# Performance work log

Hardware: AMD Instinct MI355X
Metric: run time of the kernel (lower is better)

## Reference

```python
import jax, jax.numpy as jnp
import numpy as np
import math

B, LA, LB, H = 64, 512, 512, 768


def setup_inputs() -> dict:
    key = jax.random.key(0)
    k1, k2 = jax.random.split(key)
    a = jax.random.normal(k1, (B, LA, H), dtype=jnp.float32)
    b = jax.random.normal(k2, (B, LB, H), dtype=jnp.float32)
    mask_a = jnp.ones((B, LA, 1), dtype=jnp.int32)
    mask_b = jnp.ones((B, LB, 1), dtype=jnp.int32)
    temperature = jnp.asarray(1.0 / math.sqrt(H), dtype=jnp.float32)
    return {"a": a, "b": b, "mask_a": mask_a, "mask_b": mask_b,
            "temperature": temperature}


def reference(a, b, mask_a, mask_b, temperature):
    # attn[b, i, j] = <a_i, b_j> * temperature   -> [B, LA, LB]
    attn = jnp.einsum('bih,bjh->bij', a, b) * temperature
    # pair mask: valid where both positions valid
    mask = jnp.einsum('bik,bjk->bij', mask_a.astype(jnp.float32),
                      mask_b.astype(jnp.float32)) > 0
    NEG = jnp.float32(-1e7)
    attn = jnp.where(mask, attn, NEG)
    attn_a = jax.nn.softmax(attn, axis=1)  # softmax over LA (columns normalize)
    attn_b = jax.nn.softmax(attn, axis=2)  # softmax over LB (rows normalize)
    feature_b = jnp.einsum('bij,bih->bjh', attn_a, a)  # [B, LB, H]
    feature_a = jnp.einsum('bij,bjh->bih', attn_b, b)  # [B, LA, H]
    return feature_a, feature_b
```

## Files before the change

### kernel.cpp

```cpp
#include <hip/hip_runtime.h>
#include <stdint.h>

typedef _Float16 f16;
typedef _Float16 half8_t __attribute__((ext_vector_type(8)));
typedef _Float16 half4_t __attribute__((ext_vector_type(4)));
typedef float floatx4 __attribute__((ext_vector_type(4)));

#define B_  64
#define LA_ 512
#define LB_ 512
#define H_  768

static __device__ __forceinline__ int swz(int row, int byteInRow) {
    return row * 128 + (byteInRow ^ ((row & 7) << 4));
}

__global__ __launch_bounds__(256) void qk_kernel(
    const float* __restrict__ Ag, const float* __restrict__ Bg,
    const int* __restrict__ maskA, const int* __restrict__ maskB,
    const float* __restrict__ temp_p,
    f16* __restrict__ P, f16* __restrict__ PT)
{
    __shared__ f16 As[128 * 64];
    __shared__ f16 Bs[128 * 64];
    __shared__ int mA[128];
    __shared__ int mB[128];

    const int t    = threadIdx.x;
    const int lane = t & 63;
    const int w    = t >> 6;
    const int wm   = w >> 1, wn = w & 1;
    const int jb   = blockIdx.x * 128;
    const int ib   = blockIdx.y * 128;
    const int b    = blockIdx.z;

    if (t < 128)      mA[t]       = maskA[b * LA_ + ib + t];
    else              mB[t - 128] = maskB[b * LB_ + jb + (t - 128)];

    floatx4 acc[4][4] = {};

    const int row  = t >> 1;
    const int half = t & 1;
    const float* srcA = Ag + (size_t)(b * LA_ + ib + row) * H_ + half * 32;
    const float* srcB = Bg + (size_t)(b * LB_ + jb + row) * H_ + half * 32;
    char* AsB = (char*)As;
    char* BsB = (char*)Bs;

    for (int kt = 0; kt < H_ / 64; ++kt) {
        floatx4 a4[8], b4[8];
        const floatx4* pa = (const floatx4*)(srcA + kt * 64);
        const floatx4* pb = (const floatx4*)(srcB + kt * 64);
        #pragma unroll
        for (int q = 0; q < 8; ++q) { a4[q] = pa[q]; b4[q] = pb[q]; }

        __syncthreads();
        #pragma unroll
        for (int q = 0; q < 4; ++q) {
            half8_t ha, hb;
            #pragma unroll
            for (int e = 0; e < 8; ++e) {
                ha[e] = (f16)(a4[2 * q + (e >> 2)][e & 3]);
                hb[e] = (f16)(b4[2 * q + (e >> 2)][e & 3]);
            }
            const int off = swz(row, (half * 4 + q) * 16);
            *(half8_t*)(AsB + off) = ha;
            *(half8_t*)(BsB + off) = hb;
        }
        __syncthreads();

        #pragma unroll
        for (int ks = 0; ks < 2; ++ks) {
            half8_t af[4], bf[4];
            #pragma unroll
            for (int m = 0; m < 4; ++m) {
                const int r = wm * 64 + m * 16 + (lane & 15);
                af[m] = *(half8_t*)(AsB + swz(r, ks * 64 + ((lane >> 4) << 4)));
            }
            #pragma unroll
            for (int n = 0; n < 4; ++n) {
                const int r = wn * 64 + n * 16 + (lane & 15);
                bf[n] = *(half8_t*)(BsB + swz(r, ks * 64 + ((lane >> 4) << 4)));
            }
            #pragma unroll
            for (int m = 0; m < 4; ++m)
                #pragma unroll
                for (int n = 0; n < 4; ++n)
                    acc[m][n] = __builtin_amdgcn_mfma_f32_16x16x32_f16(
                        af[m], bf[n], acc[m][n], 0, 0, 0);
        }
    }

    const float temp = *temp_p;
    #pragma unroll
    for (int m = 0; m < 4; ++m) {
        const int iloc0 = wm * 64 + m * 16 + ((lane >> 4) << 2);
        #pragma unroll
        for (int n = 0; n < 4; ++n) {
            const int jloc = wn * 64 + n * 16 + (lane & 15);
            const int vb = mB[jloc];
            half4_t hv;
            #pragma unroll
            for (int r = 0; r < 4; ++r) {
                const int iloc = iloc0 + r;
                const float s = acc[m][n][r] * temp;
                const float p = (mA[iloc] && vb) ? __expf(s) : 0.0f;
                hv[r] = (f16)p;
                P[(size_t)(b * LA_ + ib + iloc) * LB_ + jb + jloc] = hv[r];
            }
            *(half4_t*)(PT + (size_t)(b * LB_ + jb + jloc) * LA_ + ib + iloc0) = hv;
        }
    }
}

__global__ __launch_bounds__(256) void rowsum_kernel(
    const f16* __restrict__ P, const f16* __restrict__ PT,
    float* __restrict__ lrow, float* __restrict__ lcol)
{
    const int dir = blockIdx.z;
    const f16* src = dir ? PT : P;
    float*     dst = dir ? lcol : lrow;
    const int b  = blockIdx.y;
    const int rb = blockIdx.x * 64;
    const int wv = threadIdx.x >> 6, lane = threadIdx.x & 63;

    for (int r = wv; r < 64; r += 4) {
        const int row = rb + r;
        const half8_t raw = *(const half8_t*)(src + (size_t)(b * 512 + row) * 512 + lane * 8);
        float s = 0.f;
        #pragma unroll
        for (int e = 0; e < 8; ++e) s += (float)raw[e];
        #pragma unroll
        for (int off = 32; off > 0; off >>= 1) s += __shfl_down(s, off);
        if (lane == 0) dst[b * 512 + row] = s;
    }
}

__global__ __launch_bounds__(256) void pv_kernel(
    const f16* __restrict__ Pmat, const f16* __restrict__ PTmat,
    const float* __restrict__ Ag, const float* __restrict__ Bg,
    const float* __restrict__ lrow, const float* __restrict__ lcol,
    float* __restrict__ out)
{
    __shared__ f16 As[128 * 64];
    __shared__ f16 Vs[128 * 68];
    __shared__ float Sc[128];

    const int t    = threadIdx.x;
    const int lane = t & 63;
    const int w    = t >> 6;
    const int wm   = w >> 1, wn = w & 1;
    const int hb   = blockIdx.x * 128;
    const int ib   = blockIdx.y * 128;
    const int z    = blockIdx.z;
    const int dir  = z >> 6;
    const int b    = z & 63;

    const f16*   Asrc = dir ? PTmat : Pmat;
    const float* Vsrc = dir ? Ag : Bg;
    const float* lsrc = dir ? lcol : lrow;
    float* o = out + (size_t)dir * ((size_t)B_ * LA_ * H_)
                   + (size_t)(b * 512 + ib) * H_ + hb;

    if (t < 128) {
        const float l = lsrc[b * 512 + ib + t];
        Sc[t] = (l > 0.f) ? 1.0f / l : 0.0f;
    }

    floatx4 acc[4][4] = {};

    const int arow = t >> 1, ahalf = t & 1;
    const f16* aptr = Asrc + (size_t)(b * 512 + ib + arow) * 512 + ahalf * 32;
    const int jg = t >> 4, hg = t & 15;
    const float* vptr = Vsrc + (size_t)(b * 512 + jg * 4) * H_ + hb + hg * 8;

    char* AsB = (char*)As;
    char* VsB = (char*)Vs;

    for (int kt = 0; kt < 512 / 64; ++kt) {
        half8_t araw[4];
        const half8_t* pa = (const half8_t*)(aptr + kt * 64);
        #pragma unroll
        for (int q = 0; q < 4; ++q) araw[q] = pa[q];

        floatx4 vraw[4][2];
        #pragma unroll
        for (int r = 0; r < 4; ++r) {
            const floatx4* pv = (const floatx4*)(vptr + (size_t)(kt * 64 + r) * H_);
            vraw[r][0] = pv[0];
            vraw[r][1] = pv[1];
        }

        __syncthreads();
        #pragma unroll
        for (int q = 0; q < 4; ++q)
            *(half8_t*)(AsB + swz(arow, (ahalf * 4 + q) * 16)) = araw[q];

        half8_t vt[4];
        #pragma unroll
        for (int r = 0; r < 4; ++r)
            #pragma unroll
            for (int e = 0; e < 8; ++e)
                vt[r][e] = (f16)(vraw[r][e >> 2][e & 3]);
        #pragma unroll
        for (int c = 0; c < 8; ++c) {
            half4_t wv;
            wv[0] = vt[0][c]; wv[1] = vt[1][c]; wv[2] = vt[2][c]; wv[3] = vt[3][c];
            *(half4_t*)(VsB + (hg * 8 + c) * 136 + jg * 8) = wv;
        }
        __syncthreads();

        #pragma unroll
        for (int ks = 0; ks < 2; ++ks) {
            half8_t af[4], vf[4];
            #pragma unroll
            for (int m = 0; m < 4; ++m) {
                const int r = wm * 64 + m * 16 + (lane & 15);
                af[m] = *(half8_t*)(AsB + swz(r, ks * 64 + ((lane >> 4) << 4)));
            }
            #pragma unroll
            for (int n = 0; n < 4; ++n) {
                const int hr = wn * 64 + n * 16 + (lane & 15);
                const int j  = ks * 32 + ((lane >> 4) << 3);
                char* base = VsB + hr * 136 + j * 2;
                half4_t lo = *(half4_t*)base;
                half4_t hi = *(half4_t*)(base + 8);
                vf[n] = __builtin_shufflevector(lo, hi, 0, 1, 2, 3, 4, 5, 6, 7);
            }
            #pragma unroll
            for (int m = 0; m < 4; ++m)
                #pragma unroll
                for (int n = 0; n < 4; ++n)
                    acc[m][n] = __builtin_amdgcn_mfma_f32_16x16x32_f16(
                        af[m], vf[n], acc[m][n], 0, 0, 0);
        }
    }

    #pragma unroll
    for (int m = 0; m < 4; ++m) {
        const int iloc0 = wm * 64 + m * 16 + ((lane >> 4) << 2);
        #pragma unroll
        for (int n = 0; n < 4; ++n) {
            const int hloc = wn * 64 + n * 16 + (lane & 15);
            #pragma unroll
            for (int r = 0; r < 4; ++r) {
                const int iloc = iloc0 + r;
                o[(size_t)iloc * H_ + hloc] = acc[m][n][r] * Sc[iloc];
            }
        }
    }
}

extern "C" void kernel_launch(void* const* d_in, const int* in_sizes, int n_in,
                              void* d_out, int out_size, void* d_ws, size_t ws_size,
                              hipStream_t stream)
{
    const float* a    = (const float*)d_in[0];
    const float* b    = (const float*)d_in[1];
    const int*   ma   = (const int*)d_in[2];
    const int*   mb   = (const int*)d_in[3];
    const float* temp = (const float*)d_in[4];
    float*       out  = (float*)d_out;

    const size_t WS_NEEDED = 67371008;
    if (ws_size < WS_NEEDED) return;

    char* ws   = (char*)d_ws;
    f16*  P    = (f16*)ws;
    f16*  PT   = (f16*)(ws + 33554432);
    float* lrow = (float*)(ws + 67108864);
    float* lcol = (float*)(ws + 67239936);

    qk_kernel<<<dim3(LB_ / 128, LA_ / 128, B_), 256, 0, stream>>>(
        a, b, ma, mb, temp, P, PT);
    rowsum_kernel<<<dim3(512 / 64, B_, 2), 256, 0, stream>>>(P, PT, lrow, lcol);
    pv_kernel<<<dim3(H_ / 128, 512 / 128, 2 * B_), 256, 0, stream>>>(
        P, PT, a, b, lrow, lcol, out);
}
```

Measured before the change: 606.2 us.

## Pre-convert inputs to fp16 with transposes and use direct global-to-LDS loads

Adds a conversion kernel that writes fp16 copies of a and b plus transposed fp16 copies. The QK and PV GEMMs then stream these through global_load_lds 16-byte loads into the swizzled shared tiles. This removes per-tile fp32 conversion and register staging inside the GEMM loops, and in PV it removes the in-kernel transpose of V. The cost is an extra pass over the inputs and about 268 MB of workspace, and the old path is kept as a fallback when the workspace is smaller.

```diff
diff --git a/kernel.cpp b/kernel.cpp
--- a/kernel.cpp
+++ b/kernel.cpp
@@ -15,8 +15,64 @@
     return row * 128 + (byteInRow ^ ((row & 7) << 4));
 }
 
-__global__ __launch_bounds__(256) void qk_kernel(
-    const float* __restrict__ Ag, const float* __restrict__ Bg,
+static __device__ __forceinline__ void gload16(const void* g, void* l) {
+    __builtin_amdgcn_global_load_lds(
+        (const __attribute__((address_space(1))) unsigned int*)g,
+        (__attribute__((address_space(3))) unsigned int*)l,
+        16, 0, 0);
+}
+
+
+__global__ __launch_bounds__(256) void conv_kernel(
+    const float* __restrict__ A, const float* __restrict__ Bm,
+    f16* __restrict__ a16, f16* __restrict__ b16,
+    f16* __restrict__ aT, f16* __restrict__ bT)
+{
+    __shared__ f16 Ts[64][68];
+
+    const int t  = threadIdx.x;
+    const int hb = blockIdx.x * 64, lb = blockIdx.y * 64;
+    const int z  = blockIdx.z, b = z >> 1, which = z & 1;
+
+    const float* src = which ? Bm : A;
+    f16* d  = which ? b16 : a16;
+    f16* dT = which ? bT : aT;
+
+    const int r = t >> 2, cs = (t & 3) * 16;
+    const float* s = src + (size_t)(b * 512 + lb + r) * H_ + hb + cs;
+
+    f16 hv[16];
+    #pragma unroll
+    for (int q = 0; q < 4; ++q) {
+        floatx4 v = ((const floatx4*)s)[q];
+        #pragma unroll
+        for (int e = 0; e < 4; ++e) hv[q * 4 + e] = (f16)v[e];
+    }
+
+    f16* drow = d + (size_t)(b * 512 + lb + r) * H_ + hb + cs;
+    {
+        half8_t u0, u1;
+        #pragma unroll
+        for (int e = 0; e < 8; ++e) { u0[e] = hv[e]; u1[e] = hv[8 + e]; }
+        *(half8_t*)drow = u0;
+        *(half8_t*)(drow + 8) = u1;
+    }
+
+    #pragma unroll
+    for (int e = 0; e < 16; ++e) Ts[r][cs + e] = hv[e];
+    __syncthreads();
+
+    const int h = t >> 2, ls = (t & 3) * 16;
+    half8_t v0, v1;
+    #pragma unroll
+    for (int e = 0; e < 8; ++e) { v0[e] = Ts[ls + e][h]; v1[e] = Ts[ls + 8 + e][h]; }
+    f16* dTrow = dT + ((size_t)b * H_ + hb + h) * 512 + lb + ls;
+    *(half8_t*)dTrow = v0;
+    *(half8_t*)(dTrow + 8) = v1;
+}
+
+__global__ __launch_bounds__(256) void qk16_kernel(
+    const f16* __restrict__ A16, const f16* __restrict__ B16,
     const int* __restrict__ maskA, const int* __restrict__ maskB,
     const float* __restrict__ temp_p,
     f16* __restrict__ P, f16* __restrict__ PT)
@@ -39,32 +95,26 @@
 
     floatx4 acc[4][4] = {};
 
-    const int row  = t >> 1;
-    const int half = t & 1;
-    const float* srcA = Ag + (size_t)(b * LA_ + ib + row) * H_ + half * 32;
-    const float* srcB = Bg + (size_t)(b * LB_ + jb + row) * H_ + half * 32;
+    const f16* Ab = A16 + (size_t)(b * LA_ + ib) * H_;
+    const f16* Bb = B16 + (size_t)(b * LB_ + jb) * H_;
     char* AsB = (char*)As;
     char* BsB = (char*)Bs;
 
+    int srow[4], sbyt[4];
+    #pragma unroll
+    for (int q = 0; q < 4; ++q) {
+        const int o = (q * 4 + w) * 1024 + lane * 16;
+        srow[q] = o >> 7;
+        sbyt[q] = (o & 127) ^ ((srow[q] & 7) << 4);
+    }
+
     for (int kt = 0; kt < H_ / 64; ++kt) {
-        floatx4 a4[8], b4[8];
-        const floatx4* pa = (const floatx4*)(srcA + kt * 64);
-        const floatx4* pb = (const floatx4*)(srcB + kt * 64);
-        #pragma unroll
-        for (int q = 0; q < 8; ++q) { a4[q] = pa[q]; b4[q] = pb[q]; }
-
-        __syncthreads();
         #pragma unroll
         for (int q = 0; q < 4; ++q) {
-            half8_t ha, hb;
-            #pragma unroll
-            for (int e = 0; e < 8; ++e) {
-                ha[e] = (f16)(a4[2 * q + (e >> 2)][e & 3]);
-                hb[e] = (f16)(b4[2 * q + (e >> 2)][e & 3]);
-            }
-            const int off = swz(row, (half * 4 + q) * 16);
-            *(half8_t*)(AsB + off) = ha;
-            *(half8_t*)(BsB + off) = hb;
+            const int wc = q * 4 + w;
+            const size_t go = (size_t)srow[q] * H_ + kt * 64 + (sbyt[q] >> 1);
+            gload16(Ab + go, AsB + wc * 1024);
+            gload16(Bb + go, BsB + wc * 1024);
         }
         __syncthreads();
 
@@ -88,6 +138,7 @@
                     acc[m][n] = __builtin_amdgcn_mfma_f32_16x16x32_f16(
                         af[m], bf[n], acc[m][n], 0, 0, 0);
         }
+        __syncthreads();
     }
 
     const float temp = *temp_p;
@@ -135,14 +186,14 @@
     }
 }
 
-__global__ __launch_bounds__(256) void pv_kernel(
-    const f16* __restrict__ Pmat, const f16* __restrict__ PTmat,
-    const float* __restrict__ Ag, const float* __restrict__ Bg,
+__global__ __launch_bounds__(256) void pv16_kernel(
+    const f16* __restrict__ P, const f16* __restrict__ PT,
+    const f16* __restrict__ aT, const f16* __restrict__ bT,
     const float* __restrict__ lrow, const float* __restrict__ lcol,
     float* __restrict__ out)
 {
     __shared__ f16 As[128 * 64];
-    __shared__ f16 Vs[128 * 68];
+    __shared__ f16 Vs[128 * 64];
     __shared__ float Sc[128];
 
     const int t    = threadIdx.x;
@@ -155,6 +206,195 @@
     const int dir  = z >> 6;
     const int b    = z & 63;
 
+    const f16* Ab = (dir ? PT : P) + (size_t)(b * 512 + ib) * 512;
+    const f16* Vb = (dir ? aT : bT) + ((size_t)b * H_ + hb) * 512;
+    const float* lsrc = dir ? lcol : lrow;
+    float* o = out + (size_t)dir * ((size_t)B_ * LA_ * H_)
+                   + (size_t)(b * 512 + ib) * H_ + hb;
+
+    if (t < 128) {
+        const float l = lsrc[b * 512 + ib + t];
+        Sc[t] = (l > 0.f) ? 1.0f / l : 0.0f;
+    }
+
+    floatx4 acc[4][4] = {};
+    char* AsB = (char*)As;
+    char* VsB = (char*)Vs;
+
+    int srow[4], sbyt[4];
+    #pragma unroll
+    for (int q = 0; q < 4; ++q) {
+        const int o2 = (q * 4 + w) * 1024 + lane * 16;
+        srow[q] = o2 >> 7;
+        sbyt[q] = (o2 & 127) ^ ((srow[q] & 7) << 4);
+    }
+
+    for (int kt = 0; kt < 512 / 64; ++kt) {
+        #pragma unroll
+        for (int q = 0; q < 4; ++q) {
+            const int wc = q * 4 + w;
+            const size_t go = (size_t)srow[q] * 512 + kt * 64 + (sbyt[q] >> 1);
+            gload16(Ab + go, AsB + wc * 1024);
+            gload16(Vb + go, VsB + wc * 1024);
+        }
+        __syncthreads();
+
+        #pragma unroll
+        for (int ks = 0; ks < 2; ++ks) {
+            half8_t af[4], vf[4];
+            #pragma unroll
+            for (int m = 0; m < 4; ++m) {
+                const int r = wm * 64 + m * 16 + (lane & 15);
+                af[m] = *(half8_t*)(AsB + swz(r, ks * 64 + ((lane >> 4) << 4)));
+            }
+            #pragma unroll
+            for (int n = 0; n < 4; ++n) {
+                const int r = wn * 64 + n * 16 + (lane & 15);
+                vf[n] = *(half8_t*)(VsB + swz(r, ks * 64 + ((lane >> 4) << 4)));
+            }
+            #pragma unroll
+            for (int m = 0; m < 4; ++m)
+                #pragma unroll
+                for (int n = 0; n < 4; ++n)
+                    acc[m][n] = __builtin_amdgcn_mfma_f32_16x16x32_f16(
+                        af[m], vf[n], acc[m][n], 0, 0, 0);
+        }
+        __syncthreads();
+    }
+
+    #pragma unroll
+    for (int m = 0; m < 4; ++m) {
+        const int iloc0 = wm * 64 + m * 16 + ((lane >> 4) << 2);
+        #pragma unroll
+        for (int n = 0; n < 4; ++n) {
+            const int hloc = wn * 64 + n * 16 + (lane & 15);
+            #pragma unroll
+            for (int r = 0; r < 4; ++r) {
+                const int iloc = iloc0 + r;
+                o[(size_t)iloc * H_ + hloc] = acc[m][n][r] * Sc[iloc];
+            }
+        }
+    }
+}
+
+
+__global__ __launch_bounds__(256) void qk_kernel(
+    const float* __restrict__ Ag, const float* __restrict__ Bg,
+    const int* __restrict__ maskA, const int* __restrict__ maskB,
+    const float* __restrict__ temp_p,
+    f16* __restrict__ P, f16* __restrict__ PT)
+{
+    __shared__ f16 As[128 * 64];
+    __shared__ f16 Bs[128 * 64];
+    __shared__ int mA[128];
+    __shared__ int mB[128];
+
+    const int t    = threadIdx.x;
+    const int lane = t & 63;
+    const int w    = t >> 6;
+    const int wm   = w >> 1, wn = w & 1;
+    const int jb   = blockIdx.x * 128;
+    const int ib   = blockIdx.y * 128;
+    const int b    = blockIdx.z;
+
+    if (t < 128)      mA[t]       = maskA[b * LA_ + ib + t];
+    else              mB[t - 128] = maskB[b * LB_ + jb + (t - 128)];
+
+    floatx4 acc[4][4] = {};
+
+    const int row  = t >> 1;
+    const int half = t & 1;
+    const float* srcA = Ag + (size_t)(b * LA_ + ib + row) * H_ + half * 32;
+    const float* srcB = Bg + (size_t)(b * LB_ + jb + row) * H_ + half * 32;
+    char* AsB = (char*)As;
+    char* BsB = (char*)Bs;
+
+    for (int kt = 0; kt < H_ / 64; ++kt) {
+        floatx4 a4[8], b4[8];
+        const floatx4* pa = (const floatx4*)(srcA + kt * 64);
+        const floatx4* pb = (const floatx4*)(srcB + kt * 64);
+        #pragma unroll
+        for (int q = 0; q < 8; ++q) { a4[q] = pa[q]; b4[q] = pb[q]; }
+
+        __syncthreads();
+        #pragma unroll
+        for (int q = 0; q < 4; ++q) {
+            half8_t ha, hb;
+            #pragma unroll
+            for (int e = 0; e < 8; ++e) {
+                ha[e] = (f16)(a4[2 * q + (e >> 2)][e & 3]);
+                hb[e] = (f16)(b4[2 * q + (e >> 2)][e & 3]);
+            }
+            const int off = swz(row, (half * 4 + q) * 16);
+            *(half8_t*)(AsB + off) = ha;
+            *(half8_t*)(BsB + off) = hb;
+        }
+        __syncthreads();
+
+        #pragma unroll
+        for (int ks = 0; ks < 2; ++ks) {
+            half8_t af[4], bf[4];
+            #pragma unroll
+            for (int m = 0; m < 4; ++m) {
+                const int r = wm * 64 + m * 16 + (lane & 15);
+                af[m] = *(half8_t*)(AsB + swz(r, ks * 64 + ((lane >> 4) << 4)));
+            }
+            #pragma unroll
+            for (int n = 0; n < 4; ++n) {
+                const int r = wn * 64 + n * 16 + (lane & 15);
+                bf[n] = *(half8_t*)(BsB + swz(r, ks * 64 + ((lane >> 4) << 4)));
+            }
+            #pragma unroll
+            for (int m = 0; m < 4; ++m)
+                #pragma unroll
+                for (int n = 0; n < 4; ++n)
+                    acc[m][n] = __builtin_amdgcn_mfma_f32_16x16x32_f16(
+                        af[m], bf[n], acc[m][n], 0, 0, 0);
+        }
+    }
+
+    const float temp = *temp_p;
+    #pragma unroll
+    for (int m = 0; m < 4; ++m) {
+        const int iloc0 = wm * 64 + m * 16 + ((lane >> 4) << 2);
+        #pragma unroll
+        for (int n = 0; n < 4; ++n) {
+            const int jloc = wn * 64 + n * 16 + (lane & 15);
+            const int vb = mB[jloc];
+            half4_t hv;
+            #pragma unroll
+            for (int r = 0; r < 4; ++r) {
+                const int iloc = iloc0 + r;
+                const float s = acc[m][n][r] * temp;
+                const float p = (mA[iloc] && vb) ? __expf(s) : 0.0f;
+                hv[r] = (f16)p;
+                P[(size_t)(b * LA_ + ib + iloc) * LB_ + jb + jloc] = hv[r];
+            }
+            *(half4_t*)(PT + (size_t)(b * LB_ + jb + jloc) * LA_ + ib + iloc0) = hv;
+        }
+    }
+}
+
+__global__ __launch_bounds__(256) void pv_kernel(
+    const f16* __restrict__ Pmat, const f16* __restrict__ PTmat,
+    const float* __restrict__ Ag, const float* __restrict__ Bg,
+    const float* __restrict__ lrow, const float* __restrict__ lcol,
+    float* __restrict__ out)
+{
+    __shared__ f16 As[128 * 64];
+    __shared__ f16 Vs[128 * 68];
+    __shared__ float Sc[128];
+
+    const int t    = threadIdx.x;
+    const int lane = t & 63;
+    const int w    = t >> 6;
+    const int wm   = w >> 1, wn = w & 1;
+    const int hb   = blockIdx.x * 128;
+    const int ib   = blockIdx.y * 128;
+    const int z    = blockIdx.z;
+    const int dir  = z >> 6;
+    const int b    = z & 63;
+
     const f16*   Asrc = dir ? PTmat : Pmat;
     const float* Vsrc = dir ? Ag : Bg;
     const float* lsrc = dir ? lcol : lrow;
@@ -260,19 +500,38 @@
     const int*   mb   = (const int*)d_in[3];
     const float* temp = (const float*)d_in[4];
     float*       out  = (float*)d_out;
-
-    const size_t WS_NEEDED = 67371008;
-    if (ws_size < WS_NEEDED) return;
-
-    char* ws   = (char*)d_ws;
-    f16*  P    = (f16*)ws;
-    f16*  PT   = (f16*)(ws + 33554432);
-    float* lrow = (float*)(ws + 67108864);
-    float* lcol = (float*)(ws + 67239936);
-
-    qk_kernel<<<dim3(LB_ / 128, LA_ / 128, B_), 256, 0, stream>>>(
-        a, b, ma, mb, temp, P, PT);
-    rowsum_kernel<<<dim3(512 / 64, B_, 2), 256, 0, stream>>>(P, PT, lrow, lcol);
-    pv_kernel<<<dim3(H_ / 128, 512 / 128, 2 * B_), 256, 0, stream>>>(
-        P, PT, a, b, lrow, lcol, out);
-}
+    char*        ws   = (char*)d_ws;
+
+    const size_t NEW_NEED = 268697600;
+    const size_t OLD_NEED = 67371008;
+
+    if (ws_size >= NEW_NEED) {
+        f16*   a16  = (f16*)(ws);
+        f16*   b16  = (f16*)(ws + 50331648);
+        f16*   aT   = (f16*)(ws + 100663296);
+        f16*   bT   = (f16*)(ws + 150994944);
+        f16*   P    = (f16*)(ws + 201326592);
+        f16*   PT   = (f16*)(ws + 234881024);
+        float* lrow = (float*)(ws + 268435456);
+        float* lcol = (float*)(ws + 268566528);
+
+        conv_kernel<<<dim3(H_ / 64, 512 / 64, 2 * B_), 256, 0, stream>>>(
+            a, b, a16, b16, aT, bT);
+        qk16_kernel<<<dim3(LB_ / 128, LA_ / 128, B_), 256, 0, stream>>>(
+            a16, b16, ma, mb, temp, P, PT);
+        rowsum_kernel<<<dim3(512 / 64, B_, 2), 256, 0, stream>>>(P, PT, lrow, lcol);
+        pv16_kernel<<<dim3(H_ / 128, 512 / 128, 2 * B_), 256, 0, stream>>>(
+            P, PT, aT, bT, lrow, lcol, out);
+    } else if (ws_size >= OLD_NEED) {
+        f16*   P    = (f16*)(ws);
+        f16*   PT   = (f16*)(ws + 33554432);
+        float* lrow = (float*)(ws + 67108864);
+        float* lcol = (float*)(ws + 67239936);
+
+        qk_kernel<<<dim3(LB_ / 128, LA_ / 128, B_), 256, 0, stream>>>(
+            a, b, ma, mb, temp, P, PT);
+        rowsum_kernel<<<dim3(512 / 64, B_, 2), 256, 0, stream>>>(P, PT, lrow, lcol);
+        pv_kernel<<<dim3(H_ / 128, 512 / 128, 2 * B_), 256, 0, stream>>>(
+            P, PT, a, b, lrow, lcol, out);
+    }
+}
```

New measurement: 542.2 us. 10.6% less time.

## Pre-convert inputs to fp16 with transposes and double-buffer tiles via direct global-to-LDS loads

Applied to the files above, without the earlier changes.

Adds a conversion kernel that writes fp16 copies of a and b plus transposed fp16 copies. The QK and PV kernels then stream tiles straight into swizzled LDS with global_load_lds, double-buffered, with one barrier per k-step. This removes per-tile fp32 loads, conversions and the register transpose of V inside the GEMMs. Block IDs are also remapped for locality. The cost is an extra pass over the inputs and a much larger workspace requirement.

```diff
diff --git a/kernel.cpp b/kernel.cpp
--- a/kernel.cpp
+++ b/kernel.cpp
@@ -15,14 +15,69 @@
     return row * 128 + (byteInRow ^ ((row & 7) << 4));
 }
 
-__global__ __launch_bounds__(256) void qk_kernel(
-    const float* __restrict__ Ag, const float* __restrict__ Bg,
+static __device__ __forceinline__ void gload16(const void* g, void* l) {
+    __builtin_amdgcn_global_load_lds(
+        (const __attribute__((address_space(1))) unsigned int*)g,
+        (__attribute__((address_space(3))) unsigned int*)l,
+        16, 0, 0);
+}
+
+__global__ __launch_bounds__(256) void conv_kernel(
+    const float* __restrict__ A, const float* __restrict__ Bm,
+    f16* __restrict__ a16, f16* __restrict__ b16,
+    f16* __restrict__ aT, f16* __restrict__ bT)
+{
+    __shared__ f16 Ts[64][68];
+
+    const int t  = threadIdx.x;
+    const int hb = blockIdx.x * 64, lb = blockIdx.y * 64;
+    const int z  = blockIdx.z, b = z >> 1, which = z & 1;
+
+    const float* src = which ? Bm : A;
+    f16* d  = which ? b16 : a16;
+    f16* dT = which ? bT : aT;
+
+    const int r = t >> 2, cs = (t & 3) * 16;
+    const float* s = src + (size_t)(b * 512 + lb + r) * H_ + hb + cs;
+
+    f16 hv[16];
+    #pragma unroll
+    for (int q = 0; q < 4; ++q) {
+        floatx4 v = ((const floatx4*)s)[q];
+        #pragma unroll
+        for (int e = 0; e < 4; ++e) hv[q * 4 + e] = (f16)v[e];
+    }
+
+    f16* drow = d + (size_t)(b * 512 + lb + r) * H_ + hb + cs;
+    {
+        half8_t u0, u1;
+        #pragma unroll
+        for (int e = 0; e < 8; ++e) { u0[e] = hv[e]; u1[e] = hv[8 + e]; }
+        *(half8_t*)drow = u0;
+        *(half8_t*)(drow + 8) = u1;
+    }
+
+    #pragma unroll
+    for (int e = 0; e < 16; ++e) Ts[r][cs + e] = hv[e];
+    __syncthreads();
+
+    const int h = t >> 2, ls = (t & 3) * 16;
+    half8_t v0, v1;
+    #pragma unroll
+    for (int e = 0; e < 8; ++e) { v0[e] = Ts[ls + e][h]; v1[e] = Ts[ls + 8 + e][h]; }
+    f16* dTrow = dT + ((size_t)b * H_ + hb + h) * 512 + lb + ls;
+    *(half8_t*)dTrow = v0;
+    *(half8_t*)(dTrow + 8) = v1;
+}
+
+__global__ __launch_bounds__(256) void qk16_kernel(
+    const f16* __restrict__ A16, const f16* __restrict__ B16,
     const int* __restrict__ maskA, const int* __restrict__ maskB,
     const float* __restrict__ temp_p,
     f16* __restrict__ P, f16* __restrict__ PT)
 {
-    __shared__ f16 As[128 * 64];
-    __shared__ f16 Bs[128 * 64];
+    __shared__ f16 As[2][128 * 64];
+    __shared__ f16 Bs[2][128 * 64];
     __shared__ int mA[128];
     __shared__ int mB[128];
 
@@ -30,44 +85,47 @@
     const int lane = t & 63;
     const int w    = t >> 6;
     const int wm   = w >> 1, wn = w & 1;
-    const int jb   = blockIdx.x * 128;
-    const int ib   = blockIdx.y * 128;
-    const int b    = blockIdx.z;
+
+    int id = (int)blockIdx.x;
+    id = (id & 7) * 128 + (id >> 3);
+    const int jb = (id & 3) * 128;
+    const int ib = ((id >> 2) & 3) * 128;
+    const int b  = id >> 4;
 
     if (t < 128)      mA[t]       = maskA[b * LA_ + ib + t];
     else              mB[t - 128] = maskB[b * LB_ + jb + (t - 128)];
 
     floatx4 acc[4][4] = {};
 
-    const int row  = t >> 1;
-    const int half = t & 1;
-    const float* srcA = Ag + (size_t)(b * LA_ + ib + row) * H_ + half * 32;
-    const float* srcB = Bg + (size_t)(b * LB_ + jb + row) * H_ + half * 32;
-    char* AsB = (char*)As;
-    char* BsB = (char*)Bs;
+    const f16* Ab = A16 + (size_t)(b * LA_ + ib) * H_;
+    const f16* Bb = B16 + (size_t)(b * LB_ + jb) * H_;
+
+    int srow[4], sbyt[4];
+    #pragma unroll
+    for (int q = 0; q < 4; ++q) {
+        const int o = (q * 4 + w) * 1024 + lane * 16;
+        srow[q] = o >> 7;
+        sbyt[q] = (o & 127) ^ ((srow[q] & 7) << 4);
+    }
+
+    #define QK_STAGE(bufi, kt)                                            \
+        _Pragma("unroll")                                                 \
+        for (int q = 0; q < 4; ++q) {                                     \
+            const int wc = q * 4 + w;                                     \
+            const size_t go = (size_t)srow[q] * H_ + (kt) * 64 + (sbyt[q] >> 1); \
+            gload16(Ab + go, (char*)As[bufi] + wc * 1024);                \
+            gload16(Bb + go, (char*)Bs[bufi] + wc * 1024);                \
+        }
+
+    QK_STAGE(0, 0);
+    int cur = 0;
 
     for (int kt = 0; kt < H_ / 64; ++kt) {
-        floatx4 a4[8], b4[8];
-        const floatx4* pa = (const floatx4*)(srcA + kt * 64);
-        const floatx4* pb = (const floatx4*)(srcB + kt * 64);
-        #pragma unroll
-        for (int q = 0; q < 8; ++q) { a4[q] = pa[q]; b4[q] = pb[q]; }
-
         __syncthreads();
-        #pragma unroll
-        for (int q = 0; q < 4; ++q) {
-            half8_t ha, hb;
-            #pragma unroll
-            for (int e = 0; e < 8; ++e) {
-                ha[e] = (f16)(a4[2 * q + (e >> 2)][e & 3]);
-                hb[e] = (f16)(b4[2 * q + (e >> 2)][e & 3]);
-            }
-            const int off = swz(row, (half * 4 + q) * 16);
-            *(half8_t*)(AsB + off) = ha;
-            *(half8_t*)(BsB + off) = hb;
-        }
-        __syncthreads();
-
+        if (kt + 1 < H_ / 64) { QK_STAGE(cur ^ 1, kt + 1); }
+
+        char* AsB = (char*)As[cur];
+        char* BsB = (char*)Bs[cur];
         #pragma unroll
         for (int ks = 0; ks < 2; ++ks) {
             half8_t af[4], bf[4];
@@ -88,7 +146,9 @@
                     acc[m][n] = __builtin_amdgcn_mfma_f32_16x16x32_f16(
                         af[m], bf[n], acc[m][n], 0, 0, 0);
         }
-    }
+        cur ^= 1;
+    }
+    #undef QK_STAGE
 
     const float temp = *temp_p;
     #pragma unroll
@@ -135,28 +195,32 @@
     }
 }
 
-__global__ __launch_bounds__(256) void pv_kernel(
-    const f16* __restrict__ Pmat, const f16* __restrict__ PTmat,
-    const float* __restrict__ Ag, const float* __restrict__ Bg,
+__global__ __launch_bounds__(256) void pv16_kernel(
+    const f16* __restrict__ P, const f16* __restrict__ PT,
+    const f16* __restrict__ aT, const f16* __restrict__ bT,
     const float* __restrict__ lrow, const float* __restrict__ lcol,
     float* __restrict__ out)
 {
-    __shared__ f16 As[128 * 64];
-    __shared__ f16 Vs[128 * 68];
+    __shared__ f16 As[2][128 * 64];
+    __shared__ f16 Vs[2][128 * 64];
     __shared__ float Sc[128];
 
     const int t    = threadIdx.x;
     const int lane = t & 63;
     const int w    = t >> 6;
     const int wm   = w >> 1, wn = w & 1;
-    const int hb   = blockIdx.x * 128;
-    const int ib   = blockIdx.y * 128;
-    const int z    = blockIdx.z;
-    const int dir  = z >> 6;
-    const int b    = z & 63;
-
-    const f16*   Asrc = dir ? PTmat : Pmat;
-    const float* Vsrc = dir ? Ag : Bg;
+
+    int id = (int)blockIdx.x;
+    id = (id & 7) * 384 + (id >> 3);
+    const int hb = (id % 6) * 128;
+    const int rem = id / 6;
+    const int ib = (rem & 3) * 128;
+    const int z  = rem >> 2;
+    const int dir = z >> 6;
+    const int b   = z & 63;
+
+    const f16* Ab = (dir ? PT : P) + (size_t)(b * 512 + ib) * 512;
+    const f16* Vb = (dir ? aT : bT) + ((size_t)b * H_ + hb) * 512;
     const float* lsrc = dir ? lcol : lrow;
     float* o = out + (size_t)dir * ((size_t)B_ * LA_ * H_)
                    + (size_t)(b * 512 + ib) * H_ + hb;
@@ -168,47 +232,32 @@
 
     floatx4 acc[4][4] = {};
 
-    const int arow = t >> 1, ahalf = t & 1;
-    const f16* aptr = Asrc + (size_t)(b * 512 + ib + arow) * 512 + ahalf * 32;
-    const int jg = t >> 4, hg = t & 15;
-    const float* vptr = Vsrc + (size_t)(b * 512 + jg * 4) * H_ + hb + hg * 8;
-
-    char* AsB = (char*)As;
-    char* VsB = (char*)Vs;
+    int srow[4], sbyt[4];
+    #pragma unroll
+    for (int q = 0; q < 4; ++q) {
+        const int o2 = (q * 4 + w) * 1024 + lane * 16;
+        srow[q] = o2 >> 7;
+        sbyt[q] = (o2 & 127) ^ ((srow[q] & 7) << 4);
+    }
+
+    #define PV_STAGE(bufi, kt)                                            \
+        _Pragma("unroll")                                                 \
+        for (int q = 0; q < 4; ++q) {                                     \
+            const int wc = q * 4 + w;                                     \
+            const size_t go = (size_t)srow[q] * 512 + (kt) * 64 + (sbyt[q] >> 1); \
+            gload16(Ab + go, (char*)As[bufi] + wc * 1024);                \
+            gload16(Vb + go, (char*)Vs[bufi] + wc * 1024);                \
+        }
+
+    PV_STAGE(0, 0);
+    int cur = 0;
 
     for (int kt = 0; kt < 512 / 64; ++kt) {
-        half8_t araw[4];
-        const half8_t* pa = (const half8_t*)(aptr + kt * 64);
-        #pragma unroll
-        for (int q = 0; q < 4; ++q) araw[q] = pa[q];
-
-        floatx4 vraw[4][2];
-        #pragma unroll
-        for (int r = 0; r < 4; ++r) {
-            const floatx4* pv = (const floatx4*)(vptr + (size_t)(kt * 64 + r) * H_);
-            vraw[r][0] = pv[0];
-            vraw[r][1] = pv[1];
-        }
-
         __syncthreads();
-        #pragma unroll
-        for (int q = 0; q < 4; ++q)
-            *(half8_t*)(AsB + swz(arow, (ahalf * 4 + q) * 16)) = araw[q];
-
-        half8_t vt[4];
-        #pragma unroll
-        for (int r = 0; r < 4; ++r)
-            #pragma unroll
-            for (int e = 0; e < 8; ++e)
-                vt[r][e] = (f16)(vraw[r][e >> 2][e & 3]);
-        #pragma unroll
-        for (int c = 0; c < 8; ++c) {
-            half4_t wv;
-            wv[0] = vt[0][c]; wv[1] = vt[1][c]; wv[2] = vt[2][c]; wv[3] = vt[3][c];
-            *(half4_t*)(VsB + (hg * 8 + c) * 136 + jg * 8) = wv;
-        }
-        __syncthreads();
-
+        if (kt + 1 < 512 / 64) { PV_STAGE(cur ^ 1, kt + 1); }
+
+        char* AsB = (char*)As[cur];
+        char* VsB = (char*)Vs[cur];
         #pragma unroll
         for (int ks = 0; ks < 2; ++ks) {
             half8_t af[4], vf[4];
@@ -219,12 +268,8 @@
             }
             #pragma unroll
             for (int n = 0; n < 4; ++n) {
-                const int hr = wn * 64 + n * 16 + (lane & 15);
-                const int j  = ks * 32 + ((lane >> 4) << 3);
-                char* base = VsB + hr * 136 + j * 2;
-                half4_t lo = *(half4_t*)base;
-                half4_t hi = *(half4_t*)(base + 8);
-                vf[n] = __builtin_shufflevector(lo, hi, 0, 1, 2, 3, 4, 5, 6, 7);
+                const int r = wn * 64 + n * 16 + (lane & 15);
+                vf[n] = *(half8_t*)(VsB + swz(r, ks * 64 + ((lane >> 4) << 4)));
             }
             #pragma unroll
             for (int m = 0; m < 4; ++m)
@@ -233,7 +278,9 @@
                     acc[m][n] = __builtin_amdgcn_mfma_f32_16x16x32_f16(
                         af[m], vf[n], acc[m][n], 0, 0, 0);
         }
-    }
+        cur ^= 1;
+    }
+    #undef PV_STAGE
 
     #pragma unroll
     for (int m = 0; m < 4; ++m) {
@@ -260,19 +307,25 @@
     const int*   mb   = (const int*)d_in[3];
     const float* temp = (const float*)d_in[4];
     float*       out  = (float*)d_out;
-
-    const size_t WS_NEEDED = 67371008;
-    if (ws_size < WS_NEEDED) return;
-
-    char* ws   = (char*)d_ws;
-    f16*  P    = (f16*)ws;
-    f16*  PT   = (f16*)(ws + 33554432);
-    float* lrow = (float*)(ws + 67108864);
-    float* lcol = (float*)(ws + 67239936);
-
-    qk_kernel<<<dim3(LB_ / 128, LA_ / 128, B_), 256, 0, stream>>>(
-        a, b, ma, mb, temp, P, PT);
+    char*        ws   = (char*)d_ws;
+
+    const size_t NEW_NEED = 268697600;
+    if (ws_size < NEW_NEED) return;
+
+    f16*   a16  = (f16*)(ws);
+    f16*   b16  = (f16*)(ws + 50331648);
+    f16*   aT   = (f16*)(ws + 100663296);
+    f16*   bT   = (f16*)(ws + 150994944);
+    f16*   P    = (f16*)(ws + 201326592);
+    f16*   PT   = (f16*)(ws + 234881024);
+    float* lrow = (float*)(ws + 268435456);
+    float* lcol = (float*)(ws + 268566528);
+
+    conv_kernel<<<dim3(H_ / 64, 512 / 64, 2 * B_), 256, 0, stream>>>(
+        a, b, a16, b16, aT, bT);
+    qk16_kernel<<<dim3(1024, 1, 1), 256, 0, stream>>>(
+        a16, b16, ma, mb, temp, P, PT);
     rowsum_kernel<<<dim3(512 / 64, B_, 2), 256, 0, stream>>>(P, PT, lrow, lcol);
-    pv_kernel<<<dim3(H_ / 128, 512 / 128, 2 * B_), 256, 0, stream>>>(
-        P, PT, a, b, lrow, lcol, out);
-}
+    pv16_kernel<<<dim3(3072, 1, 1), 256, 0, stream>>>(
+        P, PT, aT, bT, lrow, lcol, out);
+}
```

Result: faster. 532.4 us (-12.2%).
